# Kernel optimization log

Hardware: AMD Instinct MI355X
Metric: run time of the kernel (lower is better)

## Reference

```python
import jax, jax.numpy as jnp
import numpy as np

N_NODES = 50000

def gcn_conv(x, W, b, row, col, ew, n):
    # PyG GCNConv: linear first (no bias in lin), then gcn_norm with added
    # self-loops (weight 1.0), symmetric D^{-1/2} normalization, scatter-add
    # aggregation from row (source) to col (target), then bias.
    h = x @ W                                      # [N, out]
    loop = jnp.arange(n, dtype=row.dtype)
    row_f = jnp.concatenate([row, loop])
    col_f = jnp.concatenate([col, loop])
    ew_f = jnp.concatenate([ew, jnp.ones((n,), dtype=ew.dtype)])
    deg = jax.ops.segment_sum(ew_f, col_f, num_segments=n)
    dinv = jnp.where(deg > 0, jax.lax.rsqrt(jnp.maximum(deg, 1e-30)), 0.0)
    norm = dinv[row_f] * ew_f * dinv[col_f]        # [E+N]
    msg = norm[:, None] * h[row_f]                 # gather + scale
    out = jax.ops.segment_sum(msg, col_f, num_segments=n)  # scatter-add
    return out + b

def setup_inputs() -> dict:
    key = jax.random.key(0)
    k = jax.random.split(key, 8)
    in_dim, hidden_dim, out_dim = 128, 256, 128
    n, e = N_NODES, 600000
    x = jax.random.normal(k[0], (n, in_dim), dtype=jnp.float32)
    edge_index = jax.random.randint(k[1], (2, e), 0, n, dtype=jnp.int64)
    edge_weight = jax.random.uniform(k[2], (e,), dtype=jnp.float32)
    # Glorot-style params (PyG GCNConv lin has no bias; bias added after aggregation)
    W1 = jax.random.normal(k[3], (in_dim, hidden_dim), dtype=jnp.float32) / np.sqrt(in_dim)
    b1 = jnp.zeros((hidden_dim,), dtype=jnp.float32)
    W2 = jax.random.normal(k[4], (hidden_dim, out_dim), dtype=jnp.float32) / np.sqrt(hidden_dim)
    b2 = jnp.zeros((out_dim,), dtype=jnp.float32)
    return {"x": x, "edge_index": edge_index, "edge_weight": edge_weight,
            "W1": W1, "b1": b1, "W2": W2, "b2": b2}

def reference(x, edge_index, edge_weight, W1, b1, W2, b2):
    n = x.shape[0]
    row, col = edge_index[0], edge_index[1]
    h = jax.nn.relu(gcn_conv(x, W1, b1, row, col, edge_weight, n))
    # dropout is identity in eval mode
    out = jax.nn.relu(gcn_conv(h, W2, b2, row, col, edge_weight, n))
    return out
```

## Files before the change

### kernel.cpp

```cpp
#include <hip/hip_runtime.h>
#include <hip/hip_bf16.h>

constexpr int IN_DIM  = 128;
constexpr int HID     = 256;
constexpr int OUT_DIM = 128;
constexpr int ELL_W   = 64;

typedef __attribute__((ext_vector_type(8))) short short8;
typedef __attribute__((ext_vector_type(8))) unsigned short ushort8;
typedef __attribute__((ext_vector_type(4))) float f32x4;

__device__ __forceinline__ float bf2f(unsigned short u) {
    return __uint_as_float(((unsigned int)u) << 16);
}
__device__ __forceinline__ unsigned short f2bf(float f) {
    unsigned int u = __float_as_uint(f);
    u += 0x7FFFu + ((u >> 16) & 1u);
    return (unsigned short)(u >> 16);
}
__device__ __forceinline__ unsigned short f2h(float f) {
    _Float16 h = (_Float16)f;
    unsigned short b;
    __builtin_memcpy(&b, &h, 2);
    return b;
}
__device__ __forceinline__ float h2f(unsigned short b) {
    _Float16 h;
    __builtin_memcpy(&h, &b, 2);
    return (float)h;
}
__device__ __forceinline__ unsigned int pack_e(int src, float w) {
    return (unsigned int)src | ((unsigned int)f2h(w) << 16);
}

__global__ void k_prep(int* __restrict__ cnt, int n,
                       const float* __restrict__ W1, unsigned short* __restrict__ w1t,
                       const float* __restrict__ W2, unsigned short* __restrict__ w2t) {
    const int i = blockIdx.x * 256 + threadIdx.x;
    if (i < n) cnt[i] = 0;
    if (i < IN_DIM * HID) {
        const int k = i / HID, nn = i % HID;
        w1t[(size_t)nn * IN_DIM + k] = f2bf(W1[i]);
    }
    if (i < HID * OUT_DIM) {
        const int k = i / OUT_DIM, nn = i % OUT_DIM;
        w2t[(size_t)nn * HID + k] = f2bf(W2[i]);
    }
}

__global__ void k_fill_ell(const int* __restrict__ row, const int* __restrict__ col,
                           const float* __restrict__ ew, int* __restrict__ cnt,
                           unsigned int* __restrict__ ell, int E) {
    const int i  = blockIdx.x * blockDim.x + threadIdx.x;
    const int e0 = i * 4;
    if (e0 + 3 < E) {
        const int4   c4 = *reinterpret_cast<const int4*>(col + e0);
        const int4   r4 = *reinterpret_cast<const int4*>(row + e0);
        const float4 w4 = *reinterpret_cast<const float4*>(ew + e0);
        const int p0 = atomicAdd(&cnt[c4.x], 1);
        const int p1 = atomicAdd(&cnt[c4.y], 1);
        const int p2 = atomicAdd(&cnt[c4.z], 1);
        const int p3 = atomicAdd(&cnt[c4.w], 1);
        if (p0 < ELL_W) ell[(size_t)c4.x * ELL_W + p0] = pack_e(r4.x, w4.x);
        if (p1 < ELL_W) ell[(size_t)c4.y * ELL_W + p1] = pack_e(r4.y, w4.y);
        if (p2 < ELL_W) ell[(size_t)c4.z * ELL_W + p2] = pack_e(r4.z, w4.z);
        if (p3 < ELL_W) ell[(size_t)c4.w * ELL_W + p3] = pack_e(r4.w, w4.w);
    } else {
        for (int e = e0; e < E; ++e) {
            const int c = col[e];
            const int p = atomicAdd(&cnt[c], 1);
            if (p < ELL_W) ell[(size_t)c * ELL_W + p] = pack_e(row[e], ew[e]);
        }
    }
}

__global__ __launch_bounds__(256)
void k_deg_xs(const int* __restrict__ cnt, const unsigned int* __restrict__ ell,
              const float* __restrict__ x, float* __restrict__ dinv,
              unsigned short* __restrict__ xs, int n) {
    const int wave = threadIdx.x >> 6;
    const int lane = threadIdx.x & 63;
    const int node = blockIdx.x * 4 + wave;
    if (node >= n) return;
    const int m = min(cnt[node], ELL_W);
    float s = (lane < m) ? h2f((unsigned short)(ell[(size_t)node * ELL_W + lane] >> 16)) : 0.f;
    #pragma unroll
    for (int d = 32; d; d >>= 1) s += __shfl_xor(s, d);
    const float di = rsqrtf(1.0f + s);
    if (lane == 0) dinv[node] = di;
    const float2 v = *reinterpret_cast<const float2*>(x + (size_t)node * IN_DIM + lane * 2);
    const unsigned int packed = (unsigned int)f2bf(v.x * di) |
                                ((unsigned int)f2bf(v.y * di) << 16);
    *reinterpret_cast<unsigned int*>(xs + (size_t)node * IN_DIM + lane * 2) = packed;
}

template<bool BIAS_RELU, bool BF16OUT>
__global__ __launch_bounds__(256)
void k_gather_w(const int* __restrict__ cnt, const unsigned int* __restrict__ ell,
                const float* __restrict__ dinv, const unsigned short* __restrict__ hs,
                const float* __restrict__ bias, void* __restrict__ out_, int n) {
    constexpr int F = 128;
    const int wave  = threadIdx.x >> 6;
    const int lane  = threadIdx.x & 63;
    const int group = lane >> 4;
    const int j8    = (lane & 15) * 8;
    const int node  = blockIdx.x * 4 + wave;
    if (node >= n) return;

    const int m = min(cnt[node], ELL_W);
    const unsigned int* bucket = ell + (size_t)node * ELL_W;

    float acc[8] = {};
    int p = group;
    for (; p + 4 < m; p += 8) {
        const unsigned int m0 = bucket[p], m1 = bucket[p + 4];
        const ushort8 v0 = *reinterpret_cast<const ushort8*>(hs + (size_t)(m0 & 0xFFFFu) * F + j8);
        const ushort8 v1 = *reinterpret_cast<const ushort8*>(hs + (size_t)(m1 & 0xFFFFu) * F + j8);
        const float w0 = h2f((unsigned short)(m0 >> 16));
        const float w1 = h2f((unsigned short)(m1 >> 16));
        #pragma unroll
        for (int i = 0; i < 8; ++i) acc[i] = fmaf(w0, bf2f(v0[i]), acc[i]);
        #pragma unroll
        for (int i = 0; i < 8; ++i) acc[i] = fmaf(w1, bf2f(v1[i]), acc[i]);
    }
    if (p < m) {
        const unsigned int m0 = bucket[p];
        const ushort8 v0 = *reinterpret_cast<const ushort8*>(hs + (size_t)(m0 & 0xFFFFu) * F + j8);
        const float w0 = h2f((unsigned short)(m0 >> 16));
        #pragma unroll
        for (int i = 0; i < 8; ++i) acc[i] = fmaf(w0, bf2f(v0[i]), acc[i]);
    }

    #pragma unroll
    for (int i = 0; i < 8; ++i) {
        acc[i] += __shfl_xor(acc[i], 16);
        acc[i] += __shfl_xor(acc[i], 32);
    }

    if (group == 0) {
        const float dc = dinv[node];
        const ushort8 hv = *reinterpret_cast<const ushort8*>(hs + (size_t)node * F + j8);
        float o[8];
        if (BIAS_RELU) {
            const float4 b0 = *reinterpret_cast<const float4*>(bias + j8);
            const float4 b1 = *reinterpret_cast<const float4*>(bias + j8 + 4);
            const float bb[8] = {b0.x, b0.y, b0.z, b0.w, b1.x, b1.y, b1.z, b1.w};
            #pragma unroll
            for (int i = 0; i < 8; ++i)
                o[i] = fmaxf(fmaf(dc, acc[i] + bf2f(hv[i]), bb[i]), 0.f);
        } else {
            #pragma unroll
            for (int i = 0; i < 8; ++i) o[i] = dc * (acc[i] + bf2f(hv[i]));
        }
        if (BF16OUT) {
            ushort ob[8];
            #pragma unroll
            for (int i = 0; i < 8; ++i) ob[i] = f2bf(o[i]);
            *reinterpret_cast<uint4*>((unsigned short*)out_ + (size_t)node * F + j8) =
                *reinterpret_cast<uint4*>(ob);
        } else {
            float* op = (float*)out_ + (size_t)node * F + j8;
            *reinterpret_cast<float4*>(op)     = make_float4(o[0], o[1], o[2], o[3]);
            *reinterpret_cast<float4*>(op + 4) = make_float4(o[4], o[5], o[6], o[7]);
        }
    }
}

__global__ __launch_bounds__(256)
void k_fused_gemm(const unsigned short* __restrict__ A,
                  const unsigned short* __restrict__ W1t,
                  const unsigned short* __restrict__ W2t,
                  const float* __restrict__ b1,
                  const float* __restrict__ dinv,
                  unsigned short* __restrict__ H2,
                  int M) {
    __shared__ ushort As[64 * 64];
    __shared__ ushort Bs[256 * 64];
    __shared__ ushort Hs[64 * 256];

    const int t    = threadIdx.x;
    const int w    = t >> 6;
    const int lane = t & 63;
    const int quad = lane >> 4;
    const int l16  = lane & 15;
    const int lrow = lane >> 3;
    const int lcol = ((lane & 7) ^ lrow) * 8;
    const int xr   = (l16 & 7) << 3;
    const int rowBase = blockIdx.x * 64;

    const ushort* gA  = A   + (size_t)(rowBase + w * 16 + lrow) * IN_DIM + lcol;
    const ushort* gB1 = W1t + (size_t)(w * 64 + lrow) * IN_DIM + lcol;

    f32x4 acc[4][4] = {};
    for (int k0 = 0; k0 < IN_DIM; k0 += 64) {
        #pragma unroll
        for (int j = 0; j < 2; ++j)
            __builtin_amdgcn_global_load_lds(
                (const __attribute__((address_space(1))) uint32_t*)(gA + k0 + (size_t)j * 8 * IN_DIM),
                (__attribute__((address_space(3))) uint32_t*)(&As[(w * 16 + j * 8) * 64]), 16, 0, 0);
        #pragma unroll
        for (int j = 0; j < 8; ++j)
            __builtin_amdgcn_global_load_lds(
                (const __attribute__((address_space(1))) uint32_t*)(gB1 + k0 + (size_t)j * 8 * IN_DIM),
                (__attribute__((address_space(3))) uint32_t*)(&Bs[(w * 64 + j * 8) * 64]), 16, 0, 0);
        __syncthreads();

        #pragma unroll
        for (int ks = 0; ks < 2; ++ks) {
            short8 af[4], bf[4];
            #pragma unroll
            for (int mt = 0; mt < 4; ++mt)
                af[mt] = *(const short8*)&As[(mt * 16 + l16) * 64 + ((ks * 32 + quad * 8) ^ xr)];
            #pragma unroll
            for (int nt = 0; nt < 4; ++nt)
                bf[nt] = *(const short8*)&Bs[(w * 64 + nt * 16 + l16) * 64 + ((ks * 32 + quad * 8) ^ xr)];
            #pragma unroll
            for (int mt = 0; mt < 4; ++mt)
                #pragma unroll
                for (int nt = 0; nt < 4; ++nt)
                    acc[mt][nt] = __builtin_amdgcn_mfma_f32_16x16x32_bf16(
                        af[mt], bf[nt], acc[mt][nt], 0, 0, 0);
        }
        __syncthreads();
    }

    {
        float bv[4];
        #pragma unroll
        for (int nt = 0; nt < 4; ++nt) bv[nt] = b1[w * 64 + nt * 16 + l16];
        #pragma unroll
        for (int mt = 0; mt < 4; ++mt)
            #pragma unroll
            for (int i = 0; i < 4; ++i) {
                const int row = mt * 16 + quad * 4 + i;
                const int xw  = (row & 7) << 3;
                #pragma unroll
                for (int nt = 0; nt < 4; ++nt) {
                    const int col = w * 64 + nt * 16 + l16;
                    Hs[row * 256 + (col ^ xw)] = f2bf(fmaxf(acc[mt][nt][i] + bv[nt], 0.f));
                }
            }
    }
    __syncthreads();

    const ushort* gB2 = W2t + (size_t)(w * 32 + lrow) * HID + lcol;
    f32x4 acc2[4][2] = {};
    for (int k0 = 0; k0 < HID; k0 += 64) {
        #pragma unroll
        for (int j = 0; j < 4; ++j)
            __builtin_amdgcn_global_load_lds(
                (const __attribute__((address_space(1))) uint32_t*)(gB2 + k0 + (size_t)j * 8 * HID),
                (__attribute__((address_space(3))) uint32_t*)(&Bs[(w * 32 + j * 8) * 64]), 16, 0, 0);
        __syncthreads();

        #pragma unroll
        for (int ks = 0; ks < 2; ++ks) {
            short8 af[4], bf[2];
            #pragma unroll
            for (int mt = 0; mt < 4; ++mt)
                af[mt] = *(const short8*)&Hs[(mt * 16 + l16) * 256 + ((k0 + ks * 32 + quad * 8) ^ xr)];
            #pragma unroll
            for (int nt = 0; nt < 2; ++nt)
                bf[nt] = *(const short8*)&Bs[(w * 32 + nt * 16 + l16) * 64 + ((ks * 32 + quad * 8) ^ xr)];
            #pragma unroll
            for (int mt = 0; mt < 4; ++mt)
                #pragma unroll
                for (int nt = 0; nt < 2; ++nt)
                    acc2[mt][nt] = __builtin_amdgcn_mfma_f32_16x16x32_bf16(
                        af[mt], bf[nt], acc2[mt][nt], 0, 0, 0);
        }
        __syncthreads();
    }

    #pragma unroll
    for (int mt = 0; mt < 4; ++mt)
        #pragma unroll
        for (int i = 0; i < 4; ++i) {
            const int r = rowBase + mt * 16 + quad * 4 + i;
            if (r < M) {
                const float dr = dinv[r];
                #pragma unroll
                for (int nt = 0; nt < 2; ++nt) {
                    const int c = w * 32 + nt * 16 + l16;
                    H2[(size_t)r * OUT_DIM + c] = f2bf(acc2[mt][nt][i] * dr);
                }
            }
        }
}

extern "C" void kernel_launch(void* const* d_in, const int* in_sizes, int n_in,
                              void* d_out, int out_size, void* d_ws, size_t ws_size,
                              hipStream_t stream) {
    const float* x  = (const float*)d_in[0];
    const int*   ei = (const int*)d_in[1];
    const float* ew = (const float*)d_in[2];
    const float* W1 = (const float*)d_in[3];
    const float* b1 = (const float*)d_in[4];
    const float* W2 = (const float*)d_in[5];
    const float* b2 = (const float*)d_in[6];
    float* out = (float*)d_out;

    const int n = in_sizes[0] / IN_DIM;
    const int E = in_sizes[1] / 2;
    const int Mpad = (n + 127) & ~127;
    const int* row = ei;
    const int* col = ei + E;

    float* ws = (float*)d_ws;
    size_t o = 0;
    auto alloc = [&](size_t words) { float* p = ws + o; o += (words + 63) & ~(size_t)63; return p; };
    float* dinv = alloc(n);
    int*   cnt  = (int*)alloc(n);
    unsigned int* ell = (unsigned int*)alloc((size_t)n * ELL_W);
    unsigned short* xs   = (unsigned short*)alloc((size_t)Mpad * IN_DIM / 2);
    unsigned short* aggx = (unsigned short*)alloc((size_t)Mpad * IN_DIM / 2);
    unsigned short* h2s  = (unsigned short*)alloc((size_t)Mpad * OUT_DIM / 2);
    unsigned short* w1t  = (unsigned short*)alloc((size_t)IN_DIM * HID / 2);
    unsigned short* w2t  = (unsigned short*)alloc((size_t)HID * OUT_DIM / 2);

    k_prep<<<(n + 255) / 256, 256, 0, stream>>>(cnt, n, W1, w1t, W2, w2t);
    k_fill_ell<<<(E / 4 + 255) / 256, 256, 0, stream>>>(row, col, ew, cnt, ell, E);
    k_deg_xs<<<(n + 3) / 4, 256, 0, stream>>>(cnt, ell, x, dinv, xs, n);

    k_gather_w<false, true><<<(n + 3) / 4, 256, 0, stream>>>(cnt, ell, dinv, xs, nullptr, aggx, n);

    k_fused_gemm<<<Mpad / 64, 256, 0, stream>>>(aggx, w1t, w2t, b1, dinv, h2s, n);

    k_gather_w<true, false><<<(n + 3) / 4, 256, 0, stream>>>(cnt, ell, dinv, h2s, b2, out, n);
}
```

Baseline: 205.7 us.

## Fuse first-layer gather into GEMM kernel and use one 16-lane group per node

The layer-1 neighbour aggregation now runs inside the fused GEMM kernel and writes aggregated rows straight into shared memory. This removes the intermediate aggx buffer and one kernel launch. The gather is rewritten so each 16-lane group owns a whole node, loading bucket entries cooperatively, broadcasting them by shuffle and prefetching pairs of rows, which removes the cross-group reduction. The GEMM stages are double-buffered across the freed shared-memory buffers to overlap weight loads with MFMA work. In exchange the GEMM kernel grows in latency and shared-memory footprint, and lanes within a wave can diverge when neighbouring nodes have different degrees.

New measurement: 210.9 us. 1.03x slower.

```diff
diff --git a/kernel.cpp b/kernel.cpp
--- a/kernel.cpp
+++ b/kernel.cpp
@@ -31,6 +31,40 @@
 }
 __device__ __forceinline__ unsigned int pack_e(int src, float w) {
     return (unsigned int)src | ((unsigned int)f2h(w) << 16);
+}
+
+__device__ __forceinline__ void ell_gather_acc(
+    const unsigned int* __restrict__ bucket, int m,
+    const unsigned short* __restrict__ tab, int j8, int gw, int l16,
+    float acc[8]) {
+    for (int base = 0; base < m; base += 16) {
+        const unsigned int mt = (base + l16 < m) ? bucket[base + l16] : 0u;
+        const int c16   = min(m - base, 16);
+        const int pairs = (c16 + 1) >> 1;
+        unsigned int u0 = __shfl(mt, gw * 16 + 0);
+        unsigned int u1 = __shfl(mt, gw * 16 + 1);
+        ushort8 v0 = *(const ushort8*)&tab[(size_t)(u0 & 0xFFFFu) * 128 + j8];
+        ushort8 v1 = *(const ushort8*)&tab[(size_t)(u1 & 0xFFFFu) * 128 + j8];
+        for (int p = 1; p < pairs; ++p) {
+            const unsigned int n0 = __shfl(mt, gw * 16 + 2 * p);
+            const unsigned int n1 = __shfl(mt, gw * 16 + 2 * p + 1);
+            const ushort8 w0 = *(const ushort8*)&tab[(size_t)(n0 & 0xFFFFu) * 128 + j8];
+            const ushort8 w1 = *(const ushort8*)&tab[(size_t)(n1 & 0xFFFFu) * 128 + j8];
+            const float f0 = h2f((unsigned short)(u0 >> 16));
+            const float f1 = h2f((unsigned short)(u1 >> 16));
+            #pragma unroll
+            for (int i = 0; i < 8; ++i) acc[i] = fmaf(f0, bf2f(v0[i]), acc[i]);
+            #pragma unroll
+            for (int i = 0; i < 8; ++i) acc[i] = fmaf(f1, bf2f(v1[i]), acc[i]);
+            u0 = n0; u1 = n1; v0 = w0; v1 = w1;
+        }
+        const float f0 = h2f((unsigned short)(u0 >> 16));
+        const float f1 = h2f((unsigned short)(u1 >> 16));
+        #pragma unroll
+        for (int i = 0; i < 8; ++i) acc[i] = fmaf(f0, bf2f(v0[i]), acc[i]);
+        #pragma unroll
+        for (int i = 0; i < 8; ++i) acc[i] = fmaf(f1, bf2f(v1[i]), acc[i]);
+    }
 }
 
 __global__ void k_prep(int* __restrict__ cnt, int n,
@@ -100,83 +134,57 @@
                 const float* __restrict__ dinv, const unsigned short* __restrict__ hs,
                 const float* __restrict__ bias, void* __restrict__ out_, int n) {
     constexpr int F = 128;
-    const int wave  = threadIdx.x >> 6;
-    const int lane  = threadIdx.x & 63;
-    const int group = lane >> 4;
-    const int j8    = (lane & 15) * 8;
-    const int node  = blockIdx.x * 4 + wave;
+    const int gid  = threadIdx.x >> 4;
+    const int gw   = gid & 3;
+    const int l16  = threadIdx.x & 15;
+    const int j8   = l16 * 8;
+    const int node = blockIdx.x * 16 + gid;
     if (node >= n) return;
 
     const int m = min(cnt[node], ELL_W);
     const unsigned int* bucket = ell + (size_t)node * ELL_W;
 
     float acc[8] = {};
-    int p = group;
-    for (; p + 4 < m; p += 8) {
-        const unsigned int m0 = bucket[p], m1 = bucket[p + 4];
-        const ushort8 v0 = *reinterpret_cast<const ushort8*>(hs + (size_t)(m0 & 0xFFFFu) * F + j8);
-        const ushort8 v1 = *reinterpret_cast<const ushort8*>(hs + (size_t)(m1 & 0xFFFFu) * F + j8);
-        const float w0 = h2f((unsigned short)(m0 >> 16));
-        const float w1 = h2f((unsigned short)(m1 >> 16));
-        #pragma unroll
-        for (int i = 0; i < 8; ++i) acc[i] = fmaf(w0, bf2f(v0[i]), acc[i]);
-        #pragma unroll
-        for (int i = 0; i < 8; ++i) acc[i] = fmaf(w1, bf2f(v1[i]), acc[i]);
-    }
-    if (p < m) {
-        const unsigned int m0 = bucket[p];
-        const ushort8 v0 = *reinterpret_cast<const ushort8*>(hs + (size_t)(m0 & 0xFFFFu) * F + j8);
-        const float w0 = h2f((unsigned short)(m0 >> 16));
-        #pragma unroll
-        for (int i = 0; i < 8; ++i) acc[i] = fmaf(w0, bf2f(v0[i]), acc[i]);
-    }
-
-    #pragma unroll
-    for (int i = 0; i < 8; ++i) {
-        acc[i] += __shfl_xor(acc[i], 16);
-        acc[i] += __shfl_xor(acc[i], 32);
-    }
-
-    if (group == 0) {
-        const float dc = dinv[node];
-        const ushort8 hv = *reinterpret_cast<const ushort8*>(hs + (size_t)node * F + j8);
-        float o[8];
-        if (BIAS_RELU) {
-            const float4 b0 = *reinterpret_cast<const float4*>(bias + j8);
-            const float4 b1 = *reinterpret_cast<const float4*>(bias + j8 + 4);
-            const float bb[8] = {b0.x, b0.y, b0.z, b0.w, b1.x, b1.y, b1.z, b1.w};
-            #pragma unroll
-            for (int i = 0; i < 8; ++i)
-                o[i] = fmaxf(fmaf(dc, acc[i] + bf2f(hv[i]), bb[i]), 0.f);
-        } else {
-            #pragma unroll
-            for (int i = 0; i < 8; ++i) o[i] = dc * (acc[i] + bf2f(hv[i]));
-        }
-        if (BF16OUT) {
-            ushort ob[8];
-            #pragma unroll
-            for (int i = 0; i < 8; ++i) ob[i] = f2bf(o[i]);
-            *reinterpret_cast<uint4*>((unsigned short*)out_ + (size_t)node * F + j8) =
-                *reinterpret_cast<uint4*>(ob);
-        } else {
-            float* op = (float*)out_ + (size_t)node * F + j8;
-            *reinterpret_cast<float4*>(op)     = make_float4(o[0], o[1], o[2], o[3]);
-            *reinterpret_cast<float4*>(op + 4) = make_float4(o[4], o[5], o[6], o[7]);
-        }
+    ell_gather_acc(bucket, m, hs, j8, gw, l16, acc);
+
+    const float dc = dinv[node];
+    const ushort8 hv = *reinterpret_cast<const ushort8*>(hs + (size_t)node * F + j8);
+    float o[8];
+    if (BIAS_RELU) {
+        const float4 b0 = *reinterpret_cast<const float4*>(bias + j8);
+        const float4 b1 = *reinterpret_cast<const float4*>(bias + j8 + 4);
+        const float bb[8] = {b0.x, b0.y, b0.z, b0.w, b1.x, b1.y, b1.z, b1.w};
+        #pragma unroll
+        for (int i = 0; i < 8; ++i)
+            o[i] = fmaxf(fmaf(dc, acc[i] + bf2f(hv[i]), bb[i]), 0.f);
+    } else {
+        #pragma unroll
+        for (int i = 0; i < 8; ++i) o[i] = dc * (acc[i] + bf2f(hv[i]));
+    }
+    if (BF16OUT) {
+        unsigned short ob[8];
+        #pragma unroll
+        for (int i = 0; i < 8; ++i) ob[i] = f2bf(o[i]);
+        *reinterpret_cast<uint4*>((unsigned short*)out_ + (size_t)node * F + j8) =
+            *reinterpret_cast<uint4*>(ob);
+    } else {
+        float* op = (float*)out_ + (size_t)node * F + j8;
+        *reinterpret_cast<float4*>(op)     = make_float4(o[0], o[1], o[2], o[3]);
+        *reinterpret_cast<float4*>(op + 4) = make_float4(o[4], o[5], o[6], o[7]);
     }
 }
 
 __global__ __launch_bounds__(256)
-void k_fused_gemm(const unsigned short* __restrict__ A,
+void k_fused_gemm(const int* __restrict__ cnt, const unsigned int* __restrict__ ell,
+                  const float* __restrict__ dinv, const unsigned short* __restrict__ xs,
                   const unsigned short* __restrict__ W1t,
                   const unsigned short* __restrict__ W2t,
                   const float* __restrict__ b1,
-                  const float* __restrict__ dinv,
                   unsigned short* __restrict__ H2,
-                  int M) {
-    __shared__ ushort As[64 * 64];
-    __shared__ ushort Bs[256 * 64];
-    __shared__ ushort Hs[64 * 256];
+                  int n) {
+    __shared__ unsigned short As2[64 * 128];
+    __shared__ unsigned short Bs [256 * 64];
+    __shared__ unsigned short Hs [64 * 256];
 
     const int t    = threadIdx.x;
     const int w    = t >> 6;
@@ -188,41 +196,80 @@
     const int xr   = (l16 & 7) << 3;
     const int rowBase = blockIdx.x * 64;
 
-    const ushort* gA  = A   + (size_t)(rowBase + w * 16 + lrow) * IN_DIM + lcol;
-    const ushort* gB1 = W1t + (size_t)(w * 64 + lrow) * IN_DIM + lcol;
-
-    f32x4 acc[4][4] = {};
-    for (int k0 = 0; k0 < IN_DIM; k0 += 64) {
-        #pragma unroll
-        for (int j = 0; j < 2; ++j)
-            __builtin_amdgcn_global_load_lds(
-                (const __attribute__((address_space(1))) uint32_t*)(gA + k0 + (size_t)j * 8 * IN_DIM),
-                (__attribute__((address_space(3))) uint32_t*)(&As[(w * 16 + j * 8) * 64]), 16, 0, 0);
+    const unsigned short* gB1 = W1t + (size_t)(w * 64 + lrow) * IN_DIM + lcol;
+    const unsigned short* gB2 = W2t + (size_t)(w * 32 + lrow) * HID + lcol;
+
+    auto stageW1 = [&](unsigned short* buf, int k0) {
         #pragma unroll
         for (int j = 0; j < 8; ++j)
             __builtin_amdgcn_global_load_lds(
                 (const __attribute__((address_space(1))) uint32_t*)(gB1 + k0 + (size_t)j * 8 * IN_DIM),
-                (__attribute__((address_space(3))) uint32_t*)(&Bs[(w * 64 + j * 8) * 64]), 16, 0, 0);
-        __syncthreads();
-
+                (__attribute__((address_space(3))) uint32_t*)(&buf[(w * 64 + j * 8) * 64]), 16, 0, 0);
+    };
+    auto stageW2 = [&](unsigned short* buf, int k0) {
+        #pragma unroll
+        for (int j = 0; j < 4; ++j)
+            __builtin_amdgcn_global_load_lds(
+                (const __attribute__((address_space(1))) uint32_t*)(gB2 + k0 + (size_t)j * 8 * HID),
+                (__attribute__((address_space(3))) uint32_t*)(&buf[(w * 32 + j * 8) * 64]), 16, 0, 0);
+    };
+
+    stageW1(Bs, 0);
+
+    {
+        const int gid = t >> 4;
+        const int gw  = gid & 3;
+        const int j8  = l16 * 8;
+        for (int it = 0; it < 4; ++it) {
+            const int r    = gid * 4 + it;
+            const int node = rowBase + r;
+            const int xw   = (r & 7) << 3;
+            if (node < n) {
+                const int m = min(cnt[node], ELL_W);
+                const unsigned int* bucket = ell + (size_t)node * ELL_W;
+                float acc[8] = {};
+                ell_gather_acc(bucket, m, xs, j8, gw, l16, acc);
+                const float dc = dinv[node];
+                const ushort8 hv = *reinterpret_cast<const ushort8*>(xs + (size_t)node * IN_DIM + j8);
+                unsigned short ob[8];
+                #pragma unroll
+                for (int i = 0; i < 8; ++i) ob[i] = f2bf(dc * (acc[i] + bf2f(hv[i])));
+                *reinterpret_cast<uint4*>(&As2[r * 128 + (j8 ^ xw)]) = *reinterpret_cast<uint4*>(ob);
+            } else {
+                uint4 z = {0u, 0u, 0u, 0u};
+                *reinterpret_cast<uint4*>(&As2[r * 128 + (j8 ^ xw)]) = z;
+            }
+        }
+    }
+
+    f32x4 acc[4][4] = {};
+    auto mma1 = [&](const unsigned short* Bbuf, int k0) {
         #pragma unroll
         for (int ks = 0; ks < 2; ++ks) {
-            short8 af[4], bf[4];
+            short8 af[4], bfr[4];
             #pragma unroll
             for (int mt = 0; mt < 4; ++mt)
-                af[mt] = *(const short8*)&As[(mt * 16 + l16) * 64 + ((ks * 32 + quad * 8) ^ xr)];
+                af[mt] = *(const short8*)&As2[(mt * 16 + l16) * 128 + ((k0 + ks * 32 + quad * 8) ^ xr)];
             #pragma unroll
             for (int nt = 0; nt < 4; ++nt)
-                bf[nt] = *(const short8*)&Bs[(w * 64 + nt * 16 + l16) * 64 + ((ks * 32 + quad * 8) ^ xr)];
+                bfr[nt] = *(const short8*)&Bbuf[(w * 64 + nt * 16 + l16) * 64 + ((ks * 32 + quad * 8) ^ xr)];
             #pragma unroll
             for (int mt = 0; mt < 4; ++mt)
                 #pragma unroll
                 for (int nt = 0; nt < 4; ++nt)
                     acc[mt][nt] = __builtin_amdgcn_mfma_f32_16x16x32_bf16(
-                        af[mt], bf[nt], acc[mt][nt], 0, 0, 0);
-        }
-        __syncthreads();
-    }
+                        af[mt], bfr[nt], acc[mt][nt], 0, 0, 0);
+        }
+    };
+
+    __syncthreads();
+    stageW1(Hs, 64);
+    mma1(Bs, 0);
+    __syncthreads();
+    mma1(Hs, 64);
+    __syncthreads();
+
+    stageW2(As2, 0);
 
     {
         float bv[4];
@@ -241,43 +288,45 @@
                 }
             }
     }
-    __syncthreads();
-
-    const ushort* gB2 = W2t + (size_t)(w * 32 + lrow) * HID + lcol;
+
     f32x4 acc2[4][2] = {};
-    for (int k0 = 0; k0 < HID; k0 += 64) {
-        #pragma unroll
-        for (int j = 0; j < 4; ++j)
-            __builtin_amdgcn_global_load_lds(
-                (const __attribute__((address_space(1))) uint32_t*)(gB2 + k0 + (size_t)j * 8 * HID),
-                (__attribute__((address_space(3))) uint32_t*)(&Bs[(w * 32 + j * 8) * 64]), 16, 0, 0);
-        __syncthreads();
-
+    auto mma2 = [&](const unsigned short* Bbuf, int k0) {
         #pragma unroll
         for (int ks = 0; ks < 2; ++ks) {
-            short8 af[4], bf[2];
+            short8 af[4], bfr[2];
             #pragma unroll
             for (int mt = 0; mt < 4; ++mt)
                 af[mt] = *(const short8*)&Hs[(mt * 16 + l16) * 256 + ((k0 + ks * 32 + quad * 8) ^ xr)];
             #pragma unroll
             for (int nt = 0; nt < 2; ++nt)
-                bf[nt] = *(const short8*)&Bs[(w * 32 + nt * 16 + l16) * 64 + ((ks * 32 + quad * 8) ^ xr)];
+                bfr[nt] = *(const short8*)&Bbuf[(w * 32 + nt * 16 + l16) * 64 + ((ks * 32 + quad * 8) ^ xr)];
             #pragma unroll
             for (int mt = 0; mt < 4; ++mt)
                 #pragma unroll
                 for (int nt = 0; nt < 2; ++nt)
                     acc2[mt][nt] = __builtin_amdgcn_mfma_f32_16x16x32_bf16(
-                        af[mt], bf[nt], acc2[mt][nt], 0, 0, 0);
-        }
-        __syncthreads();
-    }
+                        af[mt], bfr[nt], acc2[mt][nt], 0, 0, 0);
+        }
+    };
+
+    __syncthreads();
+    stageW2(Bs, 64);
+    mma2(As2, 0);
+    __syncthreads();
+    stageW2(As2, 128);
+    mma2(Bs, 64);
+    __syncthreads();
+    stageW2(Bs, 192);
+    mma2(As2, 128);
+    __syncthreads();
+    mma2(Bs, 192);
 
     #pragma unroll
     for (int mt = 0; mt < 4; ++mt)
         #pragma unroll
         for (int i = 0; i < 4; ++i) {
             const int r = rowBase + mt * 16 + quad * 4 + i;
-            if (r < M) {
+            if (r < n) {
                 const float dr = dinv[r];
                 #pragma unroll
                 for (int nt = 0; nt < 2; ++nt) {
@@ -313,7 +362,6 @@
     int*   cnt  = (int*)alloc(n);
     unsigned int* ell = (unsigned int*)alloc((size_t)n * ELL_W);
     unsigned short* xs   = (unsigned short*)alloc((size_t)Mpad * IN_DIM / 2);
-    unsigned short* aggx = (unsigned short*)alloc((size_t)Mpad * IN_DIM / 2);
     unsigned short* h2s  = (unsigned short*)alloc((size_t)Mpad * OUT_DIM / 2);
     unsigned short* w1t  = (unsigned short*)alloc((size_t)IN_DIM * HID / 2);
     unsigned short* w2t  = (unsigned short*)alloc((size_t)HID * OUT_DIM / 2);
@@ -322,9 +370,7 @@
     k_fill_ell<<<(E / 4 + 255) / 256, 256, 0, stream>>>(row, col, ew, cnt, ell, E);
     k_deg_xs<<<(n + 3) / 4, 256, 0, stream>>>(cnt, ell, x, dinv, xs, n);
 
-    k_gather_w<false, true><<<(n + 3) / 4, 256, 0, stream>>>(cnt, ell, dinv, xs, nullptr, aggx, n);
-
-    k_fused_gemm<<<Mpad / 64, 256, 0, stream>>>(aggx, w1t, w2t, b1, dinv, h2s, n);
-
-    k_gather_w<true, false><<<(n + 3) / 4, 256, 0, stream>>>(cnt, ell, dinv, h2s, b2, out, n);
-}
+    k_fused_gemm<<<Mpad / 64, 256, 0, stream>>>(cnt, ell, dinv, xs, w1t, w2t, b1, h2s, n);
+
+    k_gather_w<true, false><<<(n + 15) / 16, 256, 0, stream>>>(cnt, ell, dinv, h2s, b2, out, n);
+}
```

## Give each node a 16-lane group in gather; split fused GEMM into register-weight kernels

Applied to the files above, without the earlier changes.

The gather kernel now assigns one node per 16-lane group (16 nodes per block) instead of one per wave. Neighbor indices are loaded cooperatively and broadcast with shuffles, and loads for the next four neighbors are software-pipelined ahead of the FMAs. The fused two-layer GEMM is split into two kernels that keep weight fragments in registers and double-buffer 32-row A tiles, with each block handling two tiles. The split adds a global round trip for the 256-wide hidden activations, in exchange for removing per-block weight staging through LDS and the large shared footprint of the fused kernel.

Measured after the change: 207.6 us. About the same (+1.0%).

```diff
diff --git a/kernel.cpp b/kernel.cpp
--- a/kernel.cpp
+++ b/kernel.cpp
@@ -31,6 +31,47 @@
 }
 __device__ __forceinline__ unsigned int pack_e(int src, float w) {
     return (unsigned int)src | ((unsigned int)f2h(w) << 16);
+}
+
+__device__ __forceinline__ void ell_gather_acc(
+    const unsigned int* __restrict__ bucket, int m,
+    const unsigned short* __restrict__ tab, int j8, int gw, int l16,
+    float acc[8]) {
+    for (int base = 0; base < m; base += 16) {
+        const unsigned int mt = (base + l16 < m) ? bucket[base + l16] : 0u;
+        const int c16   = min(m - base, 16);
+        const int quads = (c16 + 3) >> 2;
+        unsigned int u[4];
+        ushort8 v[4];
+        #pragma unroll
+        for (int i = 0; i < 4; ++i) {
+            u[i] = __shfl(mt, gw * 16 + i);
+            v[i] = *(const ushort8*)&tab[(size_t)(u[i] & 0xFFFFu) * 128 + j8];
+        }
+        for (int q = 1; q < quads; ++q) {
+            unsigned int nu[4];
+            ushort8 nv[4];
+            #pragma unroll
+            for (int i = 0; i < 4; ++i) {
+                nu[i] = __shfl(mt, gw * 16 + q * 4 + i);
+                nv[i] = *(const ushort8*)&tab[(size_t)(nu[i] & 0xFFFFu) * 128 + j8];
+            }
+            #pragma unroll
+            for (int i = 0; i < 4; ++i) {
+                const float f = h2f((unsigned short)(u[i] >> 16));
+                #pragma unroll
+                for (int k = 0; k < 8; ++k) acc[k] = fmaf(f, bf2f(v[i][k]), acc[k]);
+            }
+            #pragma unroll
+            for (int i = 0; i < 4; ++i) { u[i] = nu[i]; v[i] = nv[i]; }
+        }
+        #pragma unroll
+        for (int i = 0; i < 4; ++i) {
+            const float f = h2f((unsigned short)(u[i] >> 16));
+            #pragma unroll
+            for (int k = 0; k < 8; ++k) acc[k] = fmaf(f, bf2f(v[i][k]), acc[k]);
+        }
+    }
 }
 
 __global__ void k_prep(int* __restrict__ cnt, int n,
@@ -100,192 +141,244 @@
                 const float* __restrict__ dinv, const unsigned short* __restrict__ hs,
                 const float* __restrict__ bias, void* __restrict__ out_, int n) {
     constexpr int F = 128;
-    const int wave  = threadIdx.x >> 6;
-    const int lane  = threadIdx.x & 63;
-    const int group = lane >> 4;
-    const int j8    = (lane & 15) * 8;
-    const int node  = blockIdx.x * 4 + wave;
+    const int gid  = threadIdx.x >> 4;
+    const int gw   = gid & 3;
+    const int l16  = threadIdx.x & 15;
+    const int j8   = l16 * 8;
+    const int node = blockIdx.x * 16 + gid;
     if (node >= n) return;
 
     const int m = min(cnt[node], ELL_W);
     const unsigned int* bucket = ell + (size_t)node * ELL_W;
 
+    const float dc = dinv[node];
+    const ushort8 hv = *reinterpret_cast<const ushort8*>(hs + (size_t)node * F + j8);
+
     float acc[8] = {};
-    int p = group;
-    for (; p + 4 < m; p += 8) {
-        const unsigned int m0 = bucket[p], m1 = bucket[p + 4];
-        const ushort8 v0 = *reinterpret_cast<const ushort8*>(hs + (size_t)(m0 & 0xFFFFu) * F + j8);
-        const ushort8 v1 = *reinterpret_cast<const ushort8*>(hs + (size_t)(m1 & 0xFFFFu) * F + j8);
-        const float w0 = h2f((unsigned short)(m0 >> 16));
-        const float w1 = h2f((unsigned short)(m1 >> 16));
-        #pragma unroll
-        for (int i = 0; i < 8; ++i) acc[i] = fmaf(w0, bf2f(v0[i]), acc[i]);
-        #pragma unroll
-        for (int i = 0; i < 8; ++i) acc[i] = fmaf(w1, bf2f(v1[i]), acc[i]);
-    }
-    if (p < m) {
-        const unsigned int m0 = bucket[p];
-        const ushort8 v0 = *reinterpret_cast<const ushort8*>(hs + (size_t)(m0 & 0xFFFFu) * F + j8);
-        const float w0 = h2f((unsigned short)(m0 >> 16));
-        #pragma unroll
-        for (int i = 0; i < 8; ++i) acc[i] = fmaf(w0, bf2f(v0[i]), acc[i]);
-    }
-
-    #pragma unroll
-    for (int i = 0; i < 8; ++i) {
-        acc[i] += __shfl_xor(acc[i], 16);
-        acc[i] += __shfl_xor(acc[i], 32);
-    }
-
-    if (group == 0) {
-        const float dc = dinv[node];
-        const ushort8 hv = *reinterpret_cast<const ushort8*>(hs + (size_t)node * F + j8);
-        float o[8];
-        if (BIAS_RELU) {
-            const float4 b0 = *reinterpret_cast<const float4*>(bias + j8);
-            const float4 b1 = *reinterpret_cast<const float4*>(bias + j8 + 4);
-            const float bb[8] = {b0.x, b0.y, b0.z, b0.w, b1.x, b1.y, b1.z, b1.w};
-            #pragma unroll
-            for (int i = 0; i < 8; ++i)
-                o[i] = fmaxf(fmaf(dc, acc[i] + bf2f(hv[i]), bb[i]), 0.f);
-        } else {
-            #pragma unroll
-            for (int i = 0; i < 8; ++i) o[i] = dc * (acc[i] + bf2f(hv[i]));
-        }
-        if (BF16OUT) {
-            ushort ob[8];
-            #pragma unroll
-            for (int i = 0; i < 8; ++i) ob[i] = f2bf(o[i]);
-            *reinterpret_cast<uint4*>((unsigned short*)out_ + (size_t)node * F + j8) =
-                *reinterpret_cast<uint4*>(ob);
-        } else {
-            float* op = (float*)out_ + (size_t)node * F + j8;
-            *reinterpret_cast<float4*>(op)     = make_float4(o[0], o[1], o[2], o[3]);
-            *reinterpret_cast<float4*>(op + 4) = make_float4(o[4], o[5], o[6], o[7]);
-        }
+    ell_gather_acc(bucket, m, hs, j8, gw, l16, acc);
+
+    float o[8];
+    if (BIAS_RELU) {
+        const float4 b0 = *reinterpret_cast<const float4*>(bias + j8);
+        const float4 b1 = *reinterpret_cast<const float4*>(bias + j8 + 4);
+        const float bb[8] = {b0.x, b0.y, b0.z, b0.w, b1.x, b1.y, b1.z, b1.w};
+        #pragma unroll
+        for (int i = 0; i < 8; ++i)
+            o[i] = fmaxf(fmaf(dc, acc[i] + bf2f(hv[i]), bb[i]), 0.f);
+    } else {
+        #pragma unroll
+        for (int i = 0; i < 8; ++i) o[i] = dc * (acc[i] + bf2f(hv[i]));
+    }
+    if (BF16OUT) {
+        unsigned short ob[8];
+        #pragma unroll
+        for (int i = 0; i < 8; ++i) ob[i] = f2bf(o[i]);
+        *reinterpret_cast<uint4*>((unsigned short*)out_ + (size_t)node * F + j8) =
+            *reinterpret_cast<uint4*>(ob);
+    } else {
+        float* op = (float*)out_ + (size_t)node * F + j8;
+        *reinterpret_cast<float4*>(op)     = make_float4(o[0], o[1], o[2], o[3]);
+        *reinterpret_cast<float4*>(op + 4) = make_float4(o[4], o[5], o[6], o[7]);
     }
 }
 
 __global__ __launch_bounds__(256)
-void k_fused_gemm(const unsigned short* __restrict__ A,
-                  const unsigned short* __restrict__ W1t,
-                  const unsigned short* __restrict__ W2t,
-                  const float* __restrict__ b1,
-                  const float* __restrict__ dinv,
-                  unsigned short* __restrict__ H2,
-                  int M) {
-    __shared__ ushort As[64 * 64];
-    __shared__ ushort Bs[256 * 64];
-    __shared__ ushort Hs[64 * 256];
+void k_gemm1(const unsigned short* __restrict__ A,
+             const unsigned short* __restrict__ W1t,
+             const float* __restrict__ b1,
+             unsigned short* __restrict__ H1,
+             int ntiles) {
+    __shared__ unsigned short As[2][32 * 128];
+    __shared__ unsigned short Hs[32 * 256];
 
     const int t    = threadIdx.x;
     const int w    = t >> 6;
     const int lane = t & 63;
     const int quad = lane >> 4;
     const int l16  = lane & 15;
-    const int lrow = lane >> 3;
-    const int lcol = ((lane & 7) ^ lrow) * 8;
     const int xr   = (l16 & 7) << 3;
-    const int rowBase = blockIdx.x * 64;
-
-    const ushort* gA  = A   + (size_t)(rowBase + w * 16 + lrow) * IN_DIM + lcol;
-    const ushort* gB1 = W1t + (size_t)(w * 64 + lrow) * IN_DIM + lcol;
-
-    f32x4 acc[4][4] = {};
-    for (int k0 = 0; k0 < IN_DIM; k0 += 64) {
-        #pragma unroll
-        for (int j = 0; j < 2; ++j)
+
+    short8 bw[4][4];
+    #pragma unroll
+    for (int nt = 0; nt < 4; ++nt)
+        #pragma unroll
+        for (int ks = 0; ks < 4; ++ks)
+            bw[nt][ks] = *(const short8*)&W1t[(size_t)(w * 64 + nt * 16 + l16) * 128 + ks * 32 + quad * 8];
+    float bv[4];
+    #pragma unroll
+    for (int nt = 0; nt < 4; ++nt) bv[nt] = b1[w * 64 + nt * 16 + l16];
+
+    auto stage = [&](int buf, int tile) {
+        #pragma unroll
+        for (int j = 0; j < 2; ++j) {
+            const int ci = j * 256 + t;
+            const int r  = ci >> 4;
+            const int c  = (ci & 15) ^ (r & 7);
             __builtin_amdgcn_global_load_lds(
-                (const __attribute__((address_space(1))) uint32_t*)(gA + k0 + (size_t)j * 8 * IN_DIM),
-                (__attribute__((address_space(3))) uint32_t*)(&As[(w * 16 + j * 8) * 64]), 16, 0, 0);
-        #pragma unroll
-        for (int j = 0; j < 8; ++j)
-            __builtin_amdgcn_global_load_lds(
-                (const __attribute__((address_space(1))) uint32_t*)(gB1 + k0 + (size_t)j * 8 * IN_DIM),
-                (__attribute__((address_space(3))) uint32_t*)(&Bs[(w * 64 + j * 8) * 64]), 16, 0, 0);
-        __syncthreads();
-
-        #pragma unroll
-        for (int ks = 0; ks < 2; ++ks) {
-            short8 af[4], bf[4];
-            #pragma unroll
-            for (int mt = 0; mt < 4; ++mt)
-                af[mt] = *(const short8*)&As[(mt * 16 + l16) * 64 + ((ks * 32 + quad * 8) ^ xr)];
-            #pragma unroll
-            for (int nt = 0; nt < 4; ++nt)
-                bf[nt] = *(const short8*)&Bs[(w * 64 + nt * 16 + l16) * 64 + ((ks * 32 + quad * 8) ^ xr)];
-            #pragma unroll
-            for (int mt = 0; mt < 4; ++mt)
+                (const __attribute__((address_space(1))) uint32_t*)(A + ((size_t)tile * 32 + r) * 128 + c * 8),
+                (__attribute__((address_space(3))) uint32_t*)(&As[buf][ci * 8]), 16, 0, 0);
+        }
+    };
+    auto mma = [&](int buf, f32x4 (&acc)[2][4]) {
+        #pragma unroll
+        for (int ks = 0; ks < 4; ++ks) {
+            short8 af[2];
+            #pragma unroll
+            for (int mt = 0; mt < 2; ++mt)
+                af[mt] = *(const short8*)&As[buf][(mt * 16 + l16) * 128 + ((ks * 32 + quad * 8) ^ xr)];
+            #pragma unroll
+            for (int mt = 0; mt < 2; ++mt)
                 #pragma unroll
                 for (int nt = 0; nt < 4; ++nt)
                     acc[mt][nt] = __builtin_amdgcn_mfma_f32_16x16x32_bf16(
-                        af[mt], bf[nt], acc[mt][nt], 0, 0, 0);
-        }
-        __syncthreads();
-    }
-
-    {
-        float bv[4];
-        #pragma unroll
-        for (int nt = 0; nt < 4; ++nt) bv[nt] = b1[w * 64 + nt * 16 + l16];
-        #pragma unroll
-        for (int mt = 0; mt < 4; ++mt)
+                        af[mt], bw[nt][ks], acc[mt][nt], 0, 0, 0);
+        }
+    };
+    auto epi_store = [&](f32x4 (&acc)[2][4]) {
+        #pragma unroll
+        for (int mt = 0; mt < 2; ++mt)
             #pragma unroll
             for (int i = 0; i < 4; ++i) {
-                const int row = mt * 16 + quad * 4 + i;
-                const int xw  = (row & 7) << 3;
+                const int r  = mt * 16 + quad * 4 + i;
+                const int xw = (r & 7) << 3;
                 #pragma unroll
                 for (int nt = 0; nt < 4; ++nt) {
                     const int col = w * 64 + nt * 16 + l16;
-                    Hs[row * 256 + (col ^ xw)] = f2bf(fmaxf(acc[mt][nt][i] + bv[nt], 0.f));
+                    Hs[r * 256 + (col ^ xw)] = f2bf(fmaxf(acc[mt][nt][i] + bv[nt], 0.f));
                 }
             }
-    }
+    };
+    auto copy_out = [&](int tile) {
+        #pragma unroll
+        for (int j = 0; j < 4; ++j) {
+            const int ci = j * 256 + t;
+            const int r  = ci >> 5;
+            const int cr = ci & 31;
+            *(uint4*)&H1[((size_t)tile * 32 + r) * 256 + cr * 8] =
+                *(const uint4*)&Hs[r * 256 + ((cr ^ (r & 7)) * 8)];
+        }
+    };
+
+    const int t0 = blockIdx.x;
+    const int t1 = blockIdx.x + gridDim.x;
+
+    stage(0, t0);
     __syncthreads();
-
-    const ushort* gB2 = W2t + (size_t)(w * 32 + lrow) * HID + lcol;
-    f32x4 acc2[4][2] = {};
-    for (int k0 = 0; k0 < HID; k0 += 64) {
-        #pragma unroll
-        for (int j = 0; j < 4; ++j)
+    if (t1 < ntiles) stage(1, t1);
+    {
+        f32x4 acc[2][4] = {};
+        mma(0, acc);
+        epi_store(acc);
+    }
+    __syncthreads();
+    copy_out(t0);
+    if (t1 < ntiles) {
+        f32x4 acc[2][4] = {};
+        mma(1, acc);
+        __syncthreads();
+        epi_store(acc);
+        __syncthreads();
+        copy_out(t1);
+    }
+}
+
+__global__ __launch_bounds__(256)
+void k_gemm2(const unsigned short* __restrict__ H1,
+             const unsigned short* __restrict__ W2t,
+             const float* __restrict__ dinv,
+             unsigned short* __restrict__ H2,
+             int n, int ntiles) {
+    __shared__ unsigned short As[2][32 * 256];
+    __shared__ unsigned short Hs[32 * 128];
+
+    const int t    = threadIdx.x;
+    const int w    = t >> 6;
+    const int lane = t & 63;
+    const int quad = lane >> 4;
+    const int l16  = lane & 15;
+    const int xr   = (l16 & 7) << 3;
+
+    short8 bw[2][8];
+    #pragma unroll
+    for (int nt = 0; nt < 2; ++nt)
+        #pragma unroll
+        for (int ks = 0; ks < 8; ++ks)
+            bw[nt][ks] = *(const short8*)&W2t[(size_t)(w * 32 + nt * 16 + l16) * 256 + ks * 32 + quad * 8];
+
+    auto stage = [&](int buf, int tile) {
+        #pragma unroll
+        for (int j = 0; j < 4; ++j) {
+            const int ci = j * 256 + t;
+            const int r  = ci >> 5;
+            const int c  = (ci & 31) ^ (r & 7);
             __builtin_amdgcn_global_load_lds(
-                (const __attribute__((address_space(1))) uint32_t*)(gB2 + k0 + (size_t)j * 8 * HID),
-                (__attribute__((address_space(3))) uint32_t*)(&Bs[(w * 32 + j * 8) * 64]), 16, 0, 0);
-        __syncthreads();
-
-        #pragma unroll
-        for (int ks = 0; ks < 2; ++ks) {
-            short8 af[4], bf[2];
-            #pragma unroll
-            for (int mt = 0; mt < 4; ++mt)
-                af[mt] = *(const short8*)&Hs[(mt * 16 + l16) * 256 + ((k0 + ks * 32 + quad * 8) ^ xr)];
-            #pragma unroll
-            for (int nt = 0; nt < 2; ++nt)
-                bf[nt] = *(const short8*)&Bs[(w * 32 + nt * 16 + l16) * 64 + ((ks * 32 + quad * 8) ^ xr)];
-            #pragma unroll
-            for (int mt = 0; mt < 4; ++mt)
+                (const __attribute__((address_space(1))) uint32_t*)(H1 + ((size_t)tile * 32 + r) * 256 + c * 8),
+                (__attribute__((address_space(3))) uint32_t*)(&As[buf][ci * 8]), 16, 0, 0);
+        }
+    };
+    auto mma = [&](int buf, f32x4 (&acc)[2][2]) {
+        #pragma unroll
+        for (int ks = 0; ks < 8; ++ks) {
+            short8 af[2];
+            #pragma unroll
+            for (int mt = 0; mt < 2; ++mt)
+                af[mt] = *(const short8*)&As[buf][(mt * 16 + l16) * 256 + ((ks * 32 + quad * 8) ^ xr)];
+            #pragma unroll
+            for (int mt = 0; mt < 2; ++mt)
                 #pragma unroll
                 for (int nt = 0; nt < 2; ++nt)
-                    acc2[mt][nt] = __builtin_amdgcn_mfma_f32_16x16x32_bf16(
-                        af[mt], bf[nt], acc2[mt][nt], 0, 0, 0);
-        }
-        __syncthreads();
-    }
-
-    #pragma unroll
-    for (int mt = 0; mt < 4; ++mt)
-        #pragma unroll
-        for (int i = 0; i < 4; ++i) {
-            const int r = rowBase + mt * 16 + quad * 4 + i;
-            if (r < M) {
-                const float dr = dinv[r];
+                    acc[mt][nt] = __builtin_amdgcn_mfma_f32_16x16x32_bf16(
+                        af[mt], bw[nt][ks], acc[mt][nt], 0, 0, 0);
+        }
+    };
+    auto epi_store = [&](f32x4 (&acc)[2][2], int tile) {
+        #pragma unroll
+        for (int mt = 0; mt < 2; ++mt)
+            #pragma unroll
+            for (int i = 0; i < 4; ++i) {
+                const int r  = mt * 16 + quad * 4 + i;
+                const int rg = tile * 32 + r;
+                const float dr = (rg < n) ? dinv[rg] : 0.f;
+                const int xw = (r & 7) << 3;
                 #pragma unroll
                 for (int nt = 0; nt < 2; ++nt) {
-                    const int c = w * 32 + nt * 16 + l16;
-                    H2[(size_t)r * OUT_DIM + c] = f2bf(acc2[mt][nt][i] * dr);
+                    const int col = w * 32 + nt * 16 + l16;
+                    Hs[r * 128 + (col ^ xw)] = f2bf(acc[mt][nt][i] * dr);
                 }
             }
-        }
+    };
+    auto copy_out = [&](int tile) {
+        #pragma unroll
+        for (int j = 0; j < 2; ++j) {
+            const int ci = j * 256 + t;
+            const int r  = ci >> 4;
+            const int cr = ci & 15;
+            *(uint4*)&H2[((size_t)tile * 32 + r) * 128 + cr * 8] =
+                *(const uint4*)&Hs[r * 128 + ((cr ^ (r & 7)) * 8)];
+        }
+    };
+
+    const int t0 = blockIdx.x;
+    const int t1 = blockIdx.x + gridDim.x;
+
+    stage(0, t0);
+    __syncthreads();
+    if (t1 < ntiles) stage(1, t1);
+    {
+        f32x4 acc[2][2] = {};
+        mma(0, acc);
+        epi_store(acc, t0);
+    }
+    __syncthreads();
+    copy_out(t0);
+    if (t1 < ntiles) {
+        f32x4 acc[2][2] = {};
+        mma(1, acc);
+        __syncthreads();
+        epi_store(acc, t1);
+        __syncthreads();
+        copy_out(t1);
+    }
 }
 
 extern "C" void kernel_launch(void* const* d_in, const int* in_sizes, int n_in,
@@ -303,6 +396,7 @@
     const int n = in_sizes[0] / IN_DIM;
     const int E = in_sizes[1] / 2;
     const int Mpad = (n + 127) & ~127;
+    const int ntiles = Mpad / 32;
     const int* row = ei;
     const int* col = ei + E;
 
@@ -314,6 +408,7 @@
     unsigned int* ell = (unsigned int*)alloc((size_t)n * ELL_W);
     unsigned short* xs   = (unsigned short*)alloc((size_t)Mpad * IN_DIM / 2);
     unsigned short* aggx = (unsigned short*)alloc((size_t)Mpad * IN_DIM / 2);
+    unsigned short* h1   = (unsigned short*)alloc((size_t)Mpad * HID / 2);
     unsigned short* h2s  = (unsigned short*)alloc((size_t)Mpad * OUT_DIM / 2);
     unsigned short* w1t  = (unsigned short*)alloc((size_t)IN_DIM * HID / 2);
     unsigned short* w2t  = (unsigned short*)alloc((size_t)HID * OUT_DIM / 2);
@@ -322,9 +417,10 @@
     k_fill_ell<<<(E / 4 + 255) / 256, 256, 0, stream>>>(row, col, ew, cnt, ell, E);
     k_deg_xs<<<(n + 3) / 4, 256, 0, stream>>>(cnt, ell, x, dinv, xs, n);
 
-    k_gather_w<false, true><<<(n + 3) / 4, 256, 0, stream>>>(cnt, ell, dinv, xs, nullptr, aggx, n);
-
-    k_fused_gemm<<<Mpad / 64, 256, 0, stream>>>(aggx, w1t, w2t, b1, dinv, h2s, n);
-
-    k_gather_w<true, false><<<(n + 3) / 4, 256, 0, stream>>>(cnt, ell, dinv, h2s, b2, out, n);
-}
+    k_gather_w<false, true><<<(n + 15) / 16, 256, 0, stream>>>(cnt, ell, dinv, xs, nullptr, aggx, n);
+
+    k_gemm1<<<ntiles / 2, 256, 0, stream>>>(aggx, w1t, b1, h1, ntiles);
+    k_gemm2<<<ntiles / 2, 256, 0, stream>>>(h1, w2t, dinv, h2s, n, ntiles);
+
+    k_gather_w<true, false><<<(n + 15) / 16, 256, 0, stream>>>(cnt, ell, dinv, h2s, b2, out, n);
+}
```
